# Performance work log

Hardware: AMD Instinct MI355X
Metric: run time of the kernel (lower is better)

The kernel has to match this reference:

```python
import jax, jax.numpy as jnp
import numpy as np

DIM = 384
WIN = 7
HEADS = 12
N = WIN * WIN
B_ = 4096
NW = 64


def _relative_position_index(ws: int) -> np.ndarray:
    coords = np.stack(np.meshgrid(np.arange(ws), np.arange(ws), indexing='ij'))  # (2, ws, ws)
    flat = coords.reshape(2, -1)  # (2, N)
    rel = flat[:, :, None] - flat[:, None, :]  # (2, N, N)
    rel = rel.transpose(1, 2, 0).copy()  # (N, N, 2)
    rel[:, :, 0] += ws - 1
    rel[:, :, 1] += ws - 1
    rel[:, :, 0] *= 2 * ws - 1
    return rel.sum(-1).astype(np.int32)  # (N, N)


def setup_inputs() -> dict:
    key = jax.random.key(0)
    ks = jax.random.split(key, 6)
    x = jax.random.normal(ks[0], (B_, N, DIM), dtype=jnp.float32)
    mask = jnp.zeros((NW, N, N), dtype=jnp.float32)
    bias_table = 0.02 * jax.random.normal(ks[1], ((2 * WIN - 1) ** 2, HEADS), dtype=jnp.float32)
    qkv_w = jax.random.normal(ks[2], (3 * DIM, DIM), dtype=jnp.float32) / np.sqrt(DIM)
    qkv_b = jnp.zeros((3 * DIM,), dtype=jnp.float32)
    proj_w = jax.random.normal(ks[3], (DIM, DIM), dtype=jnp.float32) / np.sqrt(DIM)
    proj_b = jnp.zeros((DIM,), dtype=jnp.float32)
    rel_index = jnp.asarray(_relative_position_index(WIN))  # (N, N) int32
    return {"x": x, "mask": mask, "bias_table": bias_table, "qkv_w": qkv_w,
            "qkv_b": qkv_b, "proj_w": proj_w, "proj_b": proj_b, "rel_index": rel_index}


def reference(x, mask, bias_table, qkv_w, qkv_b, proj_w, proj_b, rel_index):
    Bw, n, c = x.shape
    h = bias_table.shape[1]
    d = c // h
    scale = d ** (-0.5)
    # qkv projection: (Bw, n, 3, h, d)
    qkv = (x @ qkv_w.T + qkv_b).reshape(Bw, n, 3, h, d)
    qkv = jnp.transpose(qkv, (2, 0, 3, 1, 4))  # (3, Bw, h, n, d)
    q, k, v = qkv[0], qkv[1], qkv[2]
    attn = jnp.einsum('bhqd,bhkd->bhqk', q * scale, k)  # (Bw, h, n, n)
    bias = bias_table[rel_index]  # (n, n, h)
    attn = attn + jnp.transpose(bias, (2, 0, 1))[None]  # broadcast over Bw
    nW = mask.shape[0]
    attn = attn.reshape(Bw // nW, nW, h, n, n) + mask[None, :, None]
    attn = attn.reshape(Bw, h, n, n)
    attn = jax.nn.softmax(attn, axis=-1)
    out = jnp.einsum('bhqk,bhkd->bhqd', attn, v)  # (Bw, h, n, d)
    out = jnp.transpose(out, (0, 2, 1, 3)).reshape(Bw, n, c)
    return out @ proj_w.T + proj_b
```

## Files before the change

### kernel.cpp

```cpp
#include <hip/hip_runtime.h>
#include <hip/hip_bf16.h>

#define DIM   384
#define NWIN  49
#define HEADS 12
#define SCALE 0.17677669529663687f

typedef unsigned short ushort;
using bf16x8 = __attribute__((ext_vector_type(8))) short;
using u16x4  = __attribute__((ext_vector_type(4))) ushort;
using f32x4  = __attribute__((ext_vector_type(4))) float;

__device__ __forceinline__ ushort f2bf(float f) {
  unsigned u = __float_as_uint(f);
  u += 0x7fff + ((u >> 16) & 1);
  return (ushort)(u >> 16);
}

typedef __attribute__((address_space(1))) const void gas_void;
typedef __attribute__((address_space(3))) void las_void;

__device__ __forceinline__ void gload16(const ushort* g, ushort* l) {
  __builtin_amdgcn_global_load_lds((gas_void*)g, (las_void*)l, 16, 0, 0);
}

__global__ void prep_kernel(const float* __restrict__ qkv_w, const float* __restrict__ proj_w,
                            const float* __restrict__ bias_table, const int* __restrict__ rel_index,
                            const float* __restrict__ mask, const float* __restrict__ qkv_b,
                            ushort* __restrict__ wqb, ushort* __restrict__ wpb,
                            float* __restrict__ qbF, float* __restrict__ bmF) {
  int i0 = blockIdx.x * 256 + threadIdx.x;
  int stride = gridDim.x * 256;
  for (int i = i0; i < 1152 * 384; i += stride) {
    float v = qkv_w[i];
    if (i < 384 * 384) v *= SCALE;
    wqb[i] = f2bf(v);
  }
  for (int i = i0; i < 384 * 384; i += stride) wpb[i] = f2bf(proj_w[i]);
  for (int i = i0; i < 1152; i += stride) qbF[i] = qkv_b[i] * (i < 384 ? SCALE : 1.f);
  for (int i = i0; i < 64 * HEADS * 4 * 4 * 64 * 4; i += stride) {
    int r = i & 3, lane = (i >> 2) & 63, kt = (i >> 8) & 3, wq = (i >> 10) & 3;
    int hw = i >> 12;
    int h = hw % HEADS, wdx = hw / HEADS;
    int q = wq * 16 + (lane >> 4) * 4 + r;
    int key = kt * 16 + (lane & 15);
    float v;
    if (q < NWIN)
      v = (key < NWIN) ? bias_table[rel_index[q * NWIN + key] * HEADS + h]
                         + mask[wdx * (NWIN * NWIN) + q * NWIN + key]
                       : -3.0e38f;
    else
      v = 0.f;
    bmF[i] = v;
  }
}

#define WB_OFF 0
#define QS_OFF 24576
#define KS_OFF 29440
#define VT_OFF 34304
#define SMEM2_US 39040

__global__ __launch_bounds__(512, 2) void qkv_attn_kernel(
    const float* __restrict__ x, const float* __restrict__ qbF,
    const ushort* __restrict__ wqb, const float* __restrict__ bmF,
    ushort* __restrict__ aog)
{
  extern __shared__ ushort smem[];
  ushort* wb = smem + WB_OFF;

  const int blk = blockIdx.x;
  const int tid = threadIdx.x;
  const int w = tid >> 6, l = tid & 63;
  const int c = l & 15, g = l >> 4;
  const int wm = w >> 1, wn = w & 1;
  const int win = w >> 2, wq = w & 3;
  const float LOG2E = 1.4426950408889634f;

  auto stage_qkv = [&](int h, int kc, int buf) {
    #pragma unroll
    for (int s = 0; s < 3; ++s) {
      int i = s * 512 + tid;
      int n = i >> 4, g16 = i & 15;
      int grow = (n >> 5) * 384 + h * 32 + (n & 31);
      int sg = (g16 & 8) | ((g16 & 7) ^ (n & 7));
      gload16(wqb + (size_t)grow * DIM + kc * 128 + (sg << 3),
              wb + buf * 12288 + i * 8);
    }
  };

  bf16x8 areg[2][12] = {};
  auto compute_qkv = [&](int kcC, int buf, f32x4 (&acc)[2][3]) {
    const ushort* wcb = wb + buf * 12288;
    #pragma unroll
    for (int kk = 0; kk < 4; ++kk) {
      int sB = ((kk * 4 + g) ^ (c & 7)) << 3;
      #pragma unroll
      for (int nt = 0; nt < 3; ++nt) {
        int n = (wn * 3 + nt) * 16 + c;
        bf16x8 bb = *(const bf16x8*)&wcb[n * 128 + sB];
        acc[0][nt] = __builtin_amdgcn_mfma_f32_16x16x32_bf16(areg[0][kcC * 4 + kk], bb, acc[0][nt], 0, 0, 0);
        acc[1][nt] = __builtin_amdgcn_mfma_f32_16x16x32_bf16(areg[1][kcC * 4 + kk], bb, acc[1][nt], 0, 0, 0);
      }
    }
  };

  #pragma unroll
  for (int wi = 0; wi < 2; ++wi) {
    const float* xb = x + (size_t)((blk << 1) + wi) * (NWIN * DIM);
    for (int i = tid; i < 4704; i += 512) {
      float4 f = ((const float4*)xb)[i];
      int row = i / 96, c4 = i - row * 96;
      u16x4 v4 = { f2bf(f.x), f2bf(f.y), f2bf(f.z), f2bf(f.w) };
      *(u16x4*)&wb[row * 384 + c4 * 4] = v4;
    }
    __syncthreads();
    #pragma unroll
    for (int mt = 0; mt < 2; ++mt) {
      int row = wm * 32 + mt * 16 + c;
      int tok = row & 63;
      if ((row >> 6) == wi && tok < NWIN) {
        #pragma unroll
        for (int kg = 0; kg < 12; ++kg)
          areg[mt][kg] = *(const bf16x8*)&wb[tok * 384 + kg * 32 + g * 8];
      }
    }
    __syncthreads();
  }
  stage_qkv(0, 0, 0);
  stage_qkv(0, 1, 1);
  __syncthreads();

  for (int h = 0; h < HEADS; ++h) {
    f32x4 acc[2][3] = {};
    const int par = h & 1;

    compute_qkv(0, par, acc);
    __syncthreads();
    stage_qkv(h, 2, par);

    compute_qkv(1, par ^ 1, acc);
    __syncthreads();
    if (h < 11) stage_qkv(h + 1, 0, par ^ 1);

    compute_qkv(2, par, acc);
    __syncthreads();
    if (h < 11) stage_qkv(h + 1, 1, par);

    {
      int winE = wm >> 1;
      ushort* qsE = smem + QS_OFF + winE * 2432;
      ushort* ksE = smem + KS_OFF + winE * 2432;
      ushort* vtE = smem + VT_OFF + winE * 2368;
      #pragma unroll
      for (int nt = 0; nt < 3; ++nt) {
        int gnt = wn * 3 + nt;
        int which = gnt >> 1;
        int d = (gnt & 1) * 16 + c;
        float qb_ = qbF[which * 384 + h * 32 + d];
        #pragma unroll
        for (int mt = 0; mt < 2; ++mt) {
          #pragma unroll
          for (int r = 0; r < 4; ++r) {
            int tok = (wm & 1) * 32 + mt * 16 + g * 4 + r;
            float v = acc[mt][nt][r] + qb_;
            if (which == 0)      qsE[tok * 38 + d] = f2bf(v);
            else if (which == 1) ksE[tok * 38 + d] = f2bf(v);
            else                 vtE[d * 74 + tok] = f2bf(v);
          }
        }
      }
    }
    __syncthreads();

    ushort* qsw = smem + QS_OFF + win * 2432;
    ushort* ksw = smem + KS_OFF + win * 2432;
    ushort* vtw = smem + VT_OFF + win * 2368;
    const int wdx = ((blk << 1) + win) & 63;
    const f32x4* bw4 = (const f32x4*)(bmF + ((((size_t)(wdx * HEADS + h)) * 4 + wq) * 4 * 64 + l) * 4);
    f32x4 bmv[4];
    #pragma unroll
    for (int kt = 0; kt < 4; ++kt) bmv[kt] = bw4[kt * 64];

    f32x4 sacc[4] = {};
    {
      bf16x8 aq = *(const bf16x8*)&qsw[(wq * 16 + c) * 38 + g * 8];
      #pragma unroll
      for (int kt = 0; kt < 4; ++kt) {
        bf16x8 bk = *(const bf16x8*)&ksw[(kt * 16 + c) * 38 + g * 8];
        sacc[kt] = __builtin_amdgcn_mfma_f32_16x16x32_bf16(aq, bk, sacc[kt], 0, 0, 0);
      }
    }
    float p[4][4];
    #pragma unroll
    for (int r = 0; r < 4; ++r) {
      float s0 = sacc[0][r] + bmv[0][r], s1 = sacc[1][r] + bmv[1][r];
      float s2 = sacc[2][r] + bmv[2][r], s3 = sacc[3][r] + bmv[3][r];
      float mx = fmaxf(fmaxf(s0, s1), fmaxf(s2, s3));
      mx = fmaxf(mx, __shfl_xor(mx, 1, 64));
      mx = fmaxf(mx, __shfl_xor(mx, 2, 64));
      mx = fmaxf(mx, __shfl_xor(mx, 4, 64));
      mx = fmaxf(mx, __shfl_xor(mx, 8, 64));
      float p0 = __builtin_exp2f((s0 - mx) * LOG2E);
      float p1 = __builtin_exp2f((s1 - mx) * LOG2E);
      float p2 = __builtin_exp2f((s2 - mx) * LOG2E);
      float p3 = __builtin_exp2f((s3 - mx) * LOG2E);
      float sum = p0 + p1 + p2 + p3;
      sum += __shfl_xor(sum, 1, 64);
      sum += __shfl_xor(sum, 2, 64);
      sum += __shfl_xor(sum, 4, 64);
      sum += __shfl_xor(sum, 8, 64);
      float inv = 1.0f / sum;
      p[0][r] = p0 * inv; p[1][r] = p1 * inv; p[2][r] = p2 * inv; p[3][r] = p3 * inv;
    }
    f32x4 pacc[2] = {};
    #pragma unroll
    for (int kkh = 0; kkh < 2; ++kkh) {
      #pragma unroll
      for (int t = 0; t < 2; ++t) {
        int kt = kkh * 2 + t;
        #pragma unroll
        for (int r = 0; r < 4; ++r)
          qsw[(wq * 16 + g * 4 + r) * 38 + t * 16 + c] = f2bf(p[kt][r]);
      }
      bf16x8 ap = *(const bf16x8*)&qsw[(wq * 16 + c) * 38 + g * 8];
      #pragma unroll
      for (int dt = 0; dt < 2; ++dt) {
        bf16x8 bv = *(const bf16x8*)&vtw[(dt * 16 + c) * 74 + kkh * 32 + g * 8];
        pacc[dt] = __builtin_amdgcn_mfma_f32_16x16x32_bf16(ap, bv, pacc[dt], 0, 0, 0);
      }
    }
    #pragma unroll
    for (int dt = 0; dt < 2; ++dt) {
      #pragma unroll
      for (int rr = 0; rr < 4; ++rr) {
        int tok = wq * 16 + g * 4 + rr;
        if (tok < NWIN)
          aog[((size_t)((blk << 1) + win) * NWIN + tok) * DIM + h * 32 + dt * 16 + c] =
              f2bf(pacc[dt][rr]);
      }
    }
    __syncthreads();
  }
}

__global__ __launch_bounds__(256, 2) void proj_kernel(
    const ushort* __restrict__ ao, const ushort* __restrict__ wpb,
    const float* __restrict__ proj_b, float* __restrict__ out)
{
  extern __shared__ ushort sm3[];
  ushort* lA = sm3;
  ushort* lB = sm3 + 16384;

  const int blk = blockIdx.x;
  const int bM = blk / 3, bN = blk - bM * 3;
  const int m0 = bM * 128, n0 = bN * 128;
  const int tid = threadIdx.x;
  const int w = tid >> 6, l = tid & 63;
  const int c = l & 15, g = l >> 4;
  const int wm = w >> 1, wn = w & 1;

  auto stageA = [&](int kc, int buf) {
    #pragma unroll
    for (int s = 0; s < 4; ++s) {
      int i = s * 256 + tid;
      int row = i >> 3, g16 = i & 7;
      gload16(ao + (size_t)(m0 + row) * DIM + kc * 64 + ((g16 ^ (row & 7)) << 3),
              lA + buf * 8192 + i * 8);
    }
  };
  auto stageB = [&](int kc, int buf) {
    #pragma unroll
    for (int s = 0; s < 4; ++s) {
      int i = s * 256 + tid;
      int row = i >> 3, g16 = i & 7;
      gload16(wpb + (size_t)(n0 + row) * DIM + kc * 64 + ((g16 ^ (row & 7)) << 3),
              lB + buf * 8192 + i * 8);
    }
  };

  f32x4 acc[4][4] = {};
  stageA(0, 0); stageB(0, 0);
  stageA(1, 1); stageB(1, 1);
  __syncthreads();

  for (int kc = 0; kc < 6; ++kc) {
    const ushort* A = lA + (kc & 1) * 8192;
    const ushort* B = lB + (kc & 1) * 8192;
    #pragma unroll
    for (int kk = 0; kk < 2; ++kk) {
      int swz = ((kk * 4 + g) ^ (c & 7)) << 3;
      bf16x8 af[4], bfr[4];
      #pragma unroll
      for (int mt = 0; mt < 4; ++mt)
        af[mt] = *(const bf16x8*)&A[(wm * 64 + mt * 16 + c) * 64 + swz];
      #pragma unroll
      for (int nt = 0; nt < 4; ++nt)
        bfr[nt] = *(const bf16x8*)&B[(wn * 64 + nt * 16 + c) * 64 + swz];
      #pragma unroll
      for (int mt = 0; mt < 4; ++mt)
        #pragma unroll
        for (int nt = 0; nt < 4; ++nt)
          acc[mt][nt] = __builtin_amdgcn_mfma_f32_16x16x32_bf16(af[mt], bfr[nt], acc[mt][nt], 0, 0, 0);
    }
    __syncthreads();
    if (kc + 2 < 6) { stageA(kc + 2, kc & 1); stageB(kc + 2, kc & 1); }
  }

  #pragma unroll
  for (int nt = 0; nt < 4; ++nt) {
    int col = n0 + wn * 64 + nt * 16 + c;
    float pb = proj_b[col];
    #pragma unroll
    for (int mt = 0; mt < 4; ++mt) {
      #pragma unroll
      for (int r = 0; r < 4; ++r) {
        int row = m0 + wm * 64 + mt * 16 + g * 4 + r;
        out[(size_t)row * DIM + col] = acc[mt][nt][r] + pb;
      }
    }
  }
}

#define FWB_OFF 0
#define FQS_OFF 24576
#define FKS_OFF 29696
#define FVT_OFF 34816
#define FAO_OFF 39424
#define FSMEM_US 77056

__global__ __launch_bounds__(512, 2) void winattn_fused(
    const float* __restrict__ x, const float* __restrict__ qbF,
    const float* __restrict__ proj_b, const ushort* __restrict__ wqb,
    const ushort* __restrict__ wpb, const float* __restrict__ bmF,
    float* __restrict__ out)
{
  extern __shared__ ushort smem[];
  ushort* wb = smem + FWB_OFF;
  ushort* ao = smem + FAO_OFF;

  const int blk = blockIdx.x;
  const int tid = threadIdx.x;
  const int w = tid >> 6, l = tid & 63;
  const int c = l & 15, g = l >> 4;
  const int wm = w >> 1, wn = w & 1;
  const int win = w >> 2, wq = w & 3;
  const float LOG2E = 1.4426950408889634f;

  ushort* qsw = smem + FQS_OFF + win * 2560;
  ushort* ksw = smem + FKS_OFF + win * 2560;
  ushort* vtw = smem + FVT_OFF + win * 2304;
  ushort* psw = qsw;

  auto stage_qkv = [&](int h, int kc, int buf) {
    #pragma unroll
    for (int s = 0; s < 3; ++s) {
      int i = s * 512 + tid;
      int n = i >> 4, g16 = i & 15;
      int grow = (n >> 5) * 384 + h * 32 + (n & 31);
      int sg = (g16 & 8) | ((g16 & 7) ^ (n & 7));
      gload16(wqb + (size_t)grow * DIM + kc * 128 + (sg << 3), wb + buf * 12288 + i * 8);
    }
  };
  auto stage_proj = [&](int nb, int kc, int buf) {
    #pragma unroll
    for (int s = 0; s < 3; ++s) {
      int i = s * 512 + tid;
      int n = i >> 4, g16 = i & 15;
      int grow = nb * 96 + n;
      int sg = (g16 & 8) | ((g16 & 7) ^ (n & 7));
      gload16(wpb + (size_t)grow * DIM + kc * 128 + (sg << 3), wb + buf * 12288 + i * 8);
    }
  };

  bf16x8 areg[2][12] = {};
  auto compute_qkv = [&](int kcC, int buf, f32x4 (&acc)[2][3]) {
    const ushort* wcb = wb + buf * 12288;
    #pragma unroll
    for (int kk = 0; kk < 4; ++kk) {
      int sB = ((kk * 4 + g) ^ (c & 7)) << 3;
      #pragma unroll
      for (int nt = 0; nt < 3; ++nt) {
        int n = (wn * 3 + nt) * 16 + c;
        bf16x8 bb = *(const bf16x8*)&wcb[n * 128 + sB];
        acc[0][nt] = __builtin_amdgcn_mfma_f32_16x16x32_bf16(areg[0][kcC * 4 + kk], bb, acc[0][nt], 0, 0, 0);
        acc[1][nt] = __builtin_amdgcn_mfma_f32_16x16x32_bf16(areg[1][kcC * 4 + kk], bb, acc[1][nt], 0, 0, 0);
      }
    }
  };
  auto compute_proj = [&](int kcC, int buf, f32x4 (&acc)[2][3]) {
    const ushort* wcb = wb + buf * 12288;
    int r0 = wm * 32 + c;      if (r0 >= 98) r0 -= 64;
    int r1 = wm * 32 + 16 + c; if (r1 >= 98) r1 -= 64;
    #pragma unroll
    for (int kk = 0; kk < 4; ++kk) {
      int p = kcC * 16 + kk * 4 + g;
      int sw = (p ^ (c & 7)) << 3;
      bf16x8 a0 = *(const bf16x8*)&ao[r0 * 384 + sw];
      bf16x8 a1 = *(const bf16x8*)&ao[r1 * 384 + sw];
      int sB = ((kk * 4 + g) ^ (c & 7)) << 3;
      #pragma unroll
      for (int nt = 0; nt < 3; ++nt) {
        int n = (wn * 3 + nt) * 16 + c;
        bf16x8 bb = *(const bf16x8*)&wcb[n * 128 + sB];
        acc[0][nt] = __builtin_amdgcn_mfma_f32_16x16x32_bf16(a0, bb, acc[0][nt], 0, 0, 0);
        acc[1][nt] = __builtin_amdgcn_mfma_f32_16x16x32_bf16(a1, bb, acc[1][nt], 0, 0, 0);
      }
    }
  };

  stage_qkv(0, 0, 0);
  stage_qkv(0, 1, 1);
  {
    const float* xb = x + (size_t)blk * (2 * NWIN * DIM);
    for (int i = tid; i < 9408; i += 512) {
      float4 f = ((const float4*)xb)[i];
      int row = i / 96, c4 = i - row * 96;
      int k = c4 * 4;
      int gr = k >> 3;
      u16x4 v4 = { f2bf(f.x), f2bf(f.y), f2bf(f.z), f2bf(f.w) };
      *(u16x4*)&ao[row * 384 + ((gr ^ (row & 7)) << 3) + (k & 7)] = v4;
    }
  }
  __syncthreads();
  #pragma unroll
  for (int mt = 0; mt < 2; ++mt) {
    int row = wm * 32 + mt * 16 + c;
    int wi = row >> 6, tok = row & 63;
    if (tok < NWIN) {
      int ar = wi * 49 + tok;
      #pragma unroll
      for (int kg = 0; kg < 12; ++kg)
        areg[mt][kg] = *(const bf16x8*)&ao[ar * 384 + (((kg * 4 + g) ^ (ar & 7)) << 3)];
    }
  }

  for (int h = 0; h < HEADS; ++h) {
    f32x4 acc[2][3] = {};
    const int par = h & 1;
    compute_qkv(0, par, acc);
    __syncthreads();
    stage_qkv(h, 2, par);
    compute_qkv(1, par ^ 1, acc);
    __syncthreads();
    if (h < 11) stage_qkv(h + 1, 0, par ^ 1); else stage_proj(0, 0, par ^ 1);
    compute_qkv(2, par, acc);
    __syncthreads();
    if (h < 11) stage_qkv(h + 1, 1, par); else stage_proj(0, 1, par);
    {
      int winE = wm >> 1;
      ushort* qsE = smem + FQS_OFF + winE * 2560;
      ushort* ksE = smem + FKS_OFF + winE * 2560;
      ushort* vtE = smem + FVT_OFF + winE * 2304;
      #pragma unroll
      for (int nt = 0; nt < 3; ++nt) {
        int gnt = wn * 3 + nt;
        int which = gnt >> 1;
        int d = (gnt & 1) * 16 + c;
        float qb_ = qbF[which * 384 + h * 32 + d];
        #pragma unroll
        for (int mt = 0; mt < 2; ++mt) {
          #pragma unroll
          for (int r = 0; r < 4; ++r) {
            int tok = (wm & 1) * 32 + mt * 16 + g * 4 + r;
            float v = acc[mt][nt][r] + qb_;
            if (which == 0)      qsE[tok * 40 + d] = f2bf(v);
            else if (which == 1) ksE[tok * 40 + d] = f2bf(v);
            else                 vtE[d * 72 + tok] = f2bf(v);
          }
        }
      }
    }
    __syncthreads();

    const int wdx = ((blk << 1) + win) & 63;
    const f32x4* bw4 = (const f32x4*)(bmF + ((((size_t)(wdx * HEADS + h)) * 4 + wq) * 4 * 64 + l) * 4);
    f32x4 bmv[4];
    #pragma unroll
    for (int kt = 0; kt < 4; ++kt) bmv[kt] = bw4[kt * 64];

    f32x4 sacc[4] = {};
    {
      bf16x8 aq = *(const bf16x8*)&qsw[(wq * 16 + c) * 40 + g * 8];
      #pragma unroll
      for (int kt = 0; kt < 4; ++kt) {
        bf16x8 bk = *(const bf16x8*)&ksw[(kt * 16 + c) * 40 + g * 8];
        sacc[kt] = __builtin_amdgcn_mfma_f32_16x16x32_bf16(aq, bk, sacc[kt], 0, 0, 0);
      }
    }
    float p[4][4];
    #pragma unroll
    for (int r = 0; r < 4; ++r) {
      float s0 = sacc[0][r] + bmv[0][r], s1 = sacc[1][r] + bmv[1][r];
      float s2 = sacc[2][r] + bmv[2][r], s3 = sacc[3][r] + bmv[3][r];
      float mx = fmaxf(fmaxf(s0, s1), fmaxf(s2, s3));
      mx = fmaxf(mx, __shfl_xor(mx, 1, 64));
      mx = fmaxf(mx, __shfl_xor(mx, 2, 64));
      mx = fmaxf(mx, __shfl_xor(mx, 4, 64));
      mx = fmaxf(mx, __shfl_xor(mx, 8, 64));
      float p0 = __builtin_exp2f((s0 - mx) * LOG2E);
      float p1 = __builtin_exp2f((s1 - mx) * LOG2E);
      float p2 = __builtin_exp2f((s2 - mx) * LOG2E);
      float p3 = __builtin_exp2f((s3 - mx) * LOG2E);
      float sum = p0 + p1 + p2 + p3;
      sum += __shfl_xor(sum, 1, 64);
      sum += __shfl_xor(sum, 2, 64);
      sum += __shfl_xor(sum, 4, 64);
      sum += __shfl_xor(sum, 8, 64);
      float inv = 1.0f / sum;
      p[0][r] = p0 * inv; p[1][r] = p1 * inv; p[2][r] = p2 * inv; p[3][r] = p3 * inv;
    }
    f32x4 pacc2[2] = {};
    #pragma unroll
    for (int kkh = 0; kkh < 2; ++kkh) {
      #pragma unroll
      for (int t = 0; t < 2; ++t) {
        int kt = kkh * 2 + t;
        #pragma unroll
        for (int r = 0; r < 4; ++r)
          psw[(wq * 16 + g * 4 + r) * 40 + t * 16 + c] = f2bf(p[kt][r]);
      }
      bf16x8 ap = *(const bf16x8*)&psw[(wq * 16 + c) * 40 + g * 8];
      #pragma unroll
      for (int dt = 0; dt < 2; ++dt) {
        bf16x8 bv = *(const bf16x8*)&vtw[(dt * 16 + c) * 72 + kkh * 32 + g * 8];
        pacc2[dt] = __builtin_amdgcn_mfma_f32_16x16x32_bf16(ap, bv, pacc2[dt], 0, 0, 0);
      }
    }
    #pragma unroll
    for (int dt = 0; dt < 2; ++dt) {
      int gr0 = h * 4 + dt * 2 + (c >> 3);
      #pragma unroll
      for (int rr = 0; rr < 4; ++rr) {
        int tok = wq * 16 + g * 4 + rr;
        int row0 = win * 49 + tok;
        if (tok < NWIN)
          ao[row0 * 384 + (((gr0 ^ (row0 & 7)) << 3) | (c & 7))] = f2bf(pacc2[dt][rr]);
      }
    }
    __syncthreads();
  }

  __syncthreads();
  for (int nb = 0; nb < 4; ++nb) {
    f32x4 acc[2][3] = {};
    const int pb0 = (nb * 3) & 1;
    compute_proj(0, pb0, acc);
    __syncthreads();
    stage_proj(nb, 2, pb0);
    compute_proj(1, pb0 ^ 1, acc);
    __syncthreads();
    if (nb < 3) stage_proj(nb + 1, 0, pb0 ^ 1);
    compute_proj(2, pb0, acc);
    __syncthreads();
    if (nb < 3) stage_proj(nb + 1, 1, pb0);
    #pragma unroll
    for (int nt = 0; nt < 3; ++nt) {
      int col = nb * 96 + (wn * 3 + nt) * 16 + c;
      float pb = proj_b[col];
      #pragma unroll
      for (int mt = 0; mt < 2; ++mt) {
        #pragma unroll
        for (int r = 0; r < 4; ++r) {
          int mrow = wm * 32 + mt * 16 + g * 4 + r;
          if (mrow < 98) {
            int wi = mrow >= NWIN;
            int tok = mrow - (wi ? NWIN : 0);
            out[((size_t)((blk << 1) + wi) * NWIN + tok) * DIM + col] = acc[mt][nt][r] + pb;
          }
        }
      }
    }
  }
}

extern "C" void kernel_launch(void* const* d_in, const int* in_sizes, int n_in,
                              void* d_out, int out_size, void* d_ws, size_t ws_size,
                              hipStream_t stream) {
  const float* x          = (const float*)d_in[0];
  const float* mask       = (const float*)d_in[1];
  const float* bias_table = (const float*)d_in[2];
  const float* qkv_w      = (const float*)d_in[3];
  const float* qkv_b      = (const float*)d_in[4];
  const float* proj_w     = (const float*)d_in[5];
  const float* proj_b     = (const float*)d_in[6];
  const int*   rel_index  = (const int*)d_in[7];
  float* out = (float*)d_out;

  ushort* wqb = (ushort*)d_ws;
  ushort* wpb = (ushort*)((char*)d_ws + 884736);
  float*  qbF = (float*)((char*)d_ws + 1179648);
  float*  bmF = (float*)((char*)d_ws + 1184256);
  ushort* aog = (ushort*)((char*)d_ws + 13767168);
  const size_t NEED = 13767168ull + 154140672ull;

  prep_kernel<<<1024, 256, 0, stream>>>(qkv_w, proj_w, bias_table, rel_index, mask, qkv_b,
                                        wqb, wpb, qbF, bmF);

  if (ws_size >= NEED) {
    hipFuncSetAttribute((const void*)qkv_attn_kernel,
                        hipFuncAttributeMaxDynamicSharedMemorySize, SMEM2_US * 2);
    qkv_attn_kernel<<<2048, 512, SMEM2_US * 2, stream>>>(x, qbF, wqb, bmF, aog);
    hipFuncSetAttribute((const void*)proj_kernel,
                        hipFuncAttributeMaxDynamicSharedMemorySize, 65536);
    proj_kernel<<<4704, 256, 65536, stream>>>(aog, wpb, proj_b, out);
  } else {
    hipFuncSetAttribute((const void*)winattn_fused,
                        hipFuncAttributeMaxDynamicSharedMemorySize, FSMEM_US * 2);
    winattn_fused<<<2048, 512, FSMEM_US * 2, stream>>>(x, qbF, proj_b, wqb, wpb, bmF, out);
  }
}
```

Measured before the change: 937.6 us.

## Split fused QKV+attention into separate QKV GEMM, attention, and projection kernels

Result: no change. 929.7 us (-0.8%).

```diff
diff --git a/kernel.cpp b/kernel.cpp
--- a/kernel.cpp
+++ b/kernel.cpp
@@ -55,19 +55,295 @@
   }
 }
 
-#define WB_OFF 0
-#define QS_OFF 24576
-#define KS_OFF 29440
-#define VT_OFF 34304
-#define SMEM2_US 39040
-
-__global__ __launch_bounds__(512, 2) void qkv_attn_kernel(
+__global__ __launch_bounds__(256) void qkv_gemm_kernel(
     const float* __restrict__ x, const float* __restrict__ qbF,
-    const ushort* __restrict__ wqb, const float* __restrict__ bmF,
-    ushort* __restrict__ aog)
+    const ushort* __restrict__ wqb,
+    ushort* __restrict__ qg, ushort* __restrict__ kg, ushort* __restrict__ vg)
+{
+  extern __shared__ ushort smA[];
+  ushort* lA = smA;
+  ushort* lB = smA + 16384;
+
+  const int blk = blockIdx.x;
+  const int bM = blk / 9, bN = blk - bM * 9;
+  const int m0 = bM * 128, n0 = bN * 128;
+  const int which = bN / 3;
+  ushort* outw = which == 0 ? qg : (which == 1 ? kg : vg);
+  const int tid = threadIdx.x;
+  const int w = tid >> 6, l = tid & 63;
+  const int c = l & 15, g = l >> 4;
+  const int wm = w >> 1, wn = w & 1;
+
+  auto stageA = [&](int kc, int buf) {
+    #pragma unroll
+    for (int s = 0; s < 4; ++s) {
+      int i = s * 256 + tid;
+      int row = i >> 3, gc = i & 7;
+      const float4* src = (const float4*)(x + (size_t)(m0 + row) * DIM + kc * 64 + gc * 8);
+      float4 f0 = src[0], f1 = src[1];
+      ushort tmp[8] = { f2bf(f0.x), f2bf(f0.y), f2bf(f0.z), f2bf(f0.w),
+                        f2bf(f1.x), f2bf(f1.y), f2bf(f1.z), f2bf(f1.w) };
+      *(bf16x8*)&lA[buf * 8192 + row * 64 + ((gc ^ (row & 7)) << 3)] = *(bf16x8*)tmp;
+    }
+  };
+  auto stageB = [&](int kc, int buf) {
+    #pragma unroll
+    for (int s = 0; s < 4; ++s) {
+      int i = s * 256 + tid;
+      int row = i >> 3, gc = i & 7;
+      gload16(wqb + (size_t)(n0 + row) * DIM + kc * 64 + ((gc ^ (row & 7)) << 3),
+              lB + buf * 8192 + i * 8);
+    }
+  };
+
+  f32x4 acc[4][4] = {};
+  stageA(0, 0); stageB(0, 0);
+  stageA(1, 1); stageB(1, 1);
+  __syncthreads();
+
+  for (int kc = 0; kc < 6; ++kc) {
+    const ushort* A = lA + (kc & 1) * 8192;
+    const ushort* B = lB + (kc & 1) * 8192;
+    #pragma unroll
+    for (int kk = 0; kk < 2; ++kk) {
+      int swz = ((kk * 4 + g) ^ (c & 7)) << 3;
+      bf16x8 af[4], bfr[4];
+      #pragma unroll
+      for (int mt = 0; mt < 4; ++mt)
+        af[mt] = *(const bf16x8*)&A[(wm * 64 + mt * 16 + c) * 64 + swz];
+      #pragma unroll
+      for (int nt = 0; nt < 4; ++nt)
+        bfr[nt] = *(const bf16x8*)&B[(wn * 64 + nt * 16 + c) * 64 + swz];
+      #pragma unroll
+      for (int mt = 0; mt < 4; ++mt)
+        #pragma unroll
+        for (int nt = 0; nt < 4; ++nt)
+          acc[mt][nt] = __builtin_amdgcn_mfma_f32_16x16x32_bf16(af[mt], bfr[nt], acc[mt][nt], 0, 0, 0);
+    }
+    __syncthreads();
+    if (kc + 2 < 6) { stageA(kc + 2, kc & 1); stageB(kc + 2, kc & 1); }
+  }
+
+  #pragma unroll
+  for (int nt = 0; nt < 4; ++nt) {
+    int n = n0 + wn * 64 + nt * 16 + c;
+    int h = (n - which * 384) >> 5;
+    int d = n & 31;
+    float qb_ = qbF[n];
+    #pragma unroll
+    for (int mt = 0; mt < 4; ++mt) {
+      #pragma unroll
+      for (int r = 0; r < 4; ++r) {
+        int tok = m0 + wm * 64 + mt * 16 + g * 4 + r;
+        int win = tok / 49;
+        int tk = tok - win * 49;
+        outw[((size_t)(win * HEADS + h) * NWIN + tk) * 32 + d] = f2bf(acc[mt][nt][r] + qb_);
+      }
+    }
+  }
+}
+
+#define VSTR 68
+__global__ __launch_bounds__(256) void attn_kernel(
+    const ushort* __restrict__ kg, const ushort* __restrict__ vg,
+    const float* __restrict__ bmF, ushort* __restrict__ qg)
+{
+  __shared__ ushort vts[4][32 * VSTR];
+  __shared__ ushort pbs[4][16 * 36];
+
+  const int tid = threadIdx.x;
+  const int w = tid >> 6, l = tid & 63;
+  const int c = l & 15, g = l >> 4;
+  const int task = blockIdx.x * 4 + w;
+  const int win = task / 12, h = task - win * 12;
+  const int wdx = win & 63;
+  const float LOG2E = 1.4426950408889634f;
+
+  const size_t sb = (size_t)(win * HEADS + h) * (NWIN * 32);
+  ushort* qslice = qg + sb;
+  const ushort* kb = kg + sb;
+  const ushort* vb = vg + sb;
+  ushort* vt = vts[w];
+  ushort* pb = pbs[w];
+
+  bf16x8 qf[4], kf[4];
+  #pragma unroll
+  for (int t = 0; t < 4; ++t) {
+    qf[t] = *(const bf16x8*)(qslice + (t * 16 + c) * 32 + g * 8);
+    kf[t] = *(const bf16x8*)(kb + (t * 16 + c) * 32 + g * 8);
+  }
+  #pragma unroll
+  for (int it = 0; it < 25; ++it) {
+    int i = it * 64 + l;
+    if (i < NWIN * 32) vt[(i & 31) * VSTR + (i >> 5)] = vb[i];
+  }
+  for (int i = l; i < 32 * 15; i += 64) {
+    int d = i / 15, t = NWIN + (i - d * 15);
+    vt[d * VSTR + t] = 0;
+  }
+
+  const float* bmBase = bmF + (size_t)((wdx * HEADS + h) * 4) * 1024 + l * 4;
+
+  #pragma unroll
+  for (int qt = 0; qt < 4; ++qt) {
+    f32x4 sacc[4] = {};
+    #pragma unroll
+    for (int kt = 0; kt < 4; ++kt)
+      sacc[kt] = __builtin_amdgcn_mfma_f32_16x16x32_bf16(qf[qt], kf[kt], sacc[kt], 0, 0, 0);
+    const f32x4* bw4 = (const f32x4*)(bmBase + qt * 1024);
+    float p[4][4];
+    {
+      f32x4 b0 = bw4[0], b1 = bw4[64], b2 = bw4[128], b3 = bw4[192];
+      #pragma unroll
+      for (int r = 0; r < 4; ++r) {
+        float s0 = sacc[0][r] + b0[r], s1 = sacc[1][r] + b1[r];
+        float s2 = sacc[2][r] + b2[r], s3 = sacc[3][r] + b3[r];
+        float mx = fmaxf(fmaxf(s0, s1), fmaxf(s2, s3));
+        mx = fmaxf(mx, __shfl_xor(mx, 1, 64));
+        mx = fmaxf(mx, __shfl_xor(mx, 2, 64));
+        mx = fmaxf(mx, __shfl_xor(mx, 4, 64));
+        mx = fmaxf(mx, __shfl_xor(mx, 8, 64));
+        float p0 = __builtin_exp2f((s0 - mx) * LOG2E);
+        float p1 = __builtin_exp2f((s1 - mx) * LOG2E);
+        float p2 = __builtin_exp2f((s2 - mx) * LOG2E);
+        float p3 = __builtin_exp2f((s3 - mx) * LOG2E);
+        float sum = p0 + p1 + p2 + p3;
+        sum += __shfl_xor(sum, 1, 64);
+        sum += __shfl_xor(sum, 2, 64);
+        sum += __shfl_xor(sum, 4, 64);
+        sum += __shfl_xor(sum, 8, 64);
+        float inv = 1.0f / sum;
+        p[0][r] = p0 * inv; p[1][r] = p1 * inv; p[2][r] = p2 * inv; p[3][r] = p3 * inv;
+      }
+    }
+    f32x4 pacc[2] = {};
+    #pragma unroll
+    for (int kkh = 0; kkh < 2; ++kkh) {
+      #pragma unroll
+      for (int t = 0; t < 2; ++t) {
+        int kt = kkh * 2 + t;
+        #pragma unroll
+        for (int r = 0; r < 4; ++r)
+          pb[(g * 4 + r) * 36 + t * 16 + c] = f2bf(p[kt][r]);
+      }
+      bf16x8 ap = *(const bf16x8*)&pb[c * 36 + g * 8];
+      #pragma unroll
+      for (int dt = 0; dt < 2; ++dt) {
+        bf16x8 bv = *(const bf16x8*)&vt[(dt * 16 + c) * VSTR + kkh * 32 + g * 8];
+        pacc[dt] = __builtin_amdgcn_mfma_f32_16x16x32_bf16(ap, bv, pacc[dt], 0, 0, 0);
+      }
+    }
+    #pragma unroll
+    for (int dt = 0; dt < 2; ++dt) {
+      #pragma unroll
+      for (int rr = 0; rr < 4; ++rr) {
+        int tok = qt * 16 + g * 4 + rr;
+        if (tok < NWIN)
+          qslice[tok * 32 + dt * 16 + c] = f2bf(pacc[dt][rr]);
+      }
+    }
+  }
+}
+
+__global__ __launch_bounds__(256, 2) void proj_kernel(
+    const ushort* __restrict__ ao, const ushort* __restrict__ wpb,
+    const float* __restrict__ proj_b, float* __restrict__ out)
+{
+  extern __shared__ ushort sm3[];
+  ushort* lA = sm3;
+  ushort* lB = sm3 + 16384;
+
+  const int blk = blockIdx.x;
+  const int bM = blk / 3, bN = blk - bM * 3;
+  const int m0 = bM * 128, n0 = bN * 128;
+  const int tid = threadIdx.x;
+  const int w = tid >> 6, l = tid & 63;
+  const int c = l & 15, g = l >> 4;
+  const int wm = w >> 1, wn = w & 1;
+
+  auto stageA = [&](int kc, int buf) {
+    #pragma unroll
+    for (int s = 0; s < 4; ++s) {
+      int i = s * 256 + tid;
+      int row = i >> 3, gc = i & 7;
+      int tok = m0 + row;
+      int win = tok / 49;
+      int tk = tok - win * 49;
+      int sg = gc ^ (row & 7);
+      int kfull = kc * 64 + sg * 8;
+      gload16(ao + ((size_t)(win * HEADS + (kfull >> 5)) * NWIN + tk) * 32 + (kfull & 31),
+              lA + buf * 8192 + i * 8);
+    }
+  };
+  auto stageB = [&](int kc, int buf) {
+    #pragma unroll
+    for (int s = 0; s < 4; ++s) {
+      int i = s * 256 + tid;
+      int row = i >> 3, gc = i & 7;
+      gload16(wpb + (size_t)(n0 + row) * DIM + kc * 64 + ((gc ^ (row & 7)) << 3),
+              lB + buf * 8192 + i * 8);
+    }
+  };
+
+  f32x4 acc[4][4] = {};
+  stageA(0, 0); stageB(0, 0);
+  stageA(1, 1); stageB(1, 1);
+  __syncthreads();
+
+  for (int kc = 0; kc < 6; ++kc) {
+    const ushort* A = lA + (kc & 1) * 8192;
+    const ushort* B = lB + (kc & 1) * 8192;
+    #pragma unroll
+    for (int kk = 0; kk < 2; ++kk) {
+      int swz = ((kk * 4 + g) ^ (c & 7)) << 3;
+      bf16x8 af[4], bfr[4];
+      #pragma unroll
+      for (int mt = 0; mt < 4; ++mt)
+        af[mt] = *(const bf16x8*)&A[(wm * 64 + mt * 16 + c) * 64 + swz];
+      #pragma unroll
+      for (int nt = 0; nt < 4; ++nt)
+        bfr[nt] = *(const bf16x8*)&B[(wn * 64 + nt * 16 + c) * 64 + swz];
+      #pragma unroll
+      for (int mt = 0; mt < 4; ++mt)
+        #pragma unroll
+        for (int nt = 0; nt < 4; ++nt)
+          acc[mt][nt] = __builtin_amdgcn_mfma_f32_16x16x32_bf16(af[mt], bfr[nt], acc[mt][nt], 0, 0, 0);
+    }
+    __syncthreads();
+    if (kc + 2 < 6) { stageA(kc + 2, kc & 1); stageB(kc + 2, kc & 1); }
+  }
+
+  #pragma unroll
+  for (int nt = 0; nt < 4; ++nt) {
+    int col = n0 + wn * 64 + nt * 16 + c;
+    float pb = proj_b[col];
+    #pragma unroll
+    for (int mt = 0; mt < 4; ++mt) {
+      #pragma unroll
+      for (int r = 0; r < 4; ++r) {
+        int row = m0 + wm * 64 + mt * 16 + g * 4 + r;
+        out[(size_t)row * DIM + col] = acc[mt][nt][r] + pb;
+      }
+    }
+  }
+}
+
+#define FWB_OFF 0
+#define FQS_OFF 24576
+#define FKS_OFF 29696
+#define FVT_OFF 34816
+#define FAO_OFF 39424
+#define FSMEM_US 77056
+
+__global__ __launch_bounds__(512, 2) void winattn_fused(
+    const float* __restrict__ x, const float* __restrict__ qbF,
+    const float* __restrict__ proj_b, const ushort* __restrict__ wqb,
+    const ushort* __restrict__ wpb, const float* __restrict__ bmF,
+    float* __restrict__ out)
 {
   extern __shared__ ushort smem[];
-  ushort* wb = smem + WB_OFF;
+  ushort* wb = smem + FWB_OFF;
+  ushort* ao = smem + FAO_OFF;
 
   const int blk = blockIdx.x;
   const int tid = threadIdx.x;
@@ -77,6 +353,11 @@
   const int win = w >> 2, wq = w & 3;
   const float LOG2E = 1.4426950408889634f;
 
+  ushort* qsw = smem + FQS_OFF + win * 2560;
+  ushort* ksw = smem + FKS_OFF + win * 2560;
+  ushort* vtw = smem + FVT_OFF + win * 2304;
+  ushort* psw = qsw;
+
   auto stage_qkv = [&](int h, int kc, int buf) {
     #pragma unroll
     for (int s = 0; s < 3; ++s) {
@@ -84,8 +365,17 @@
       int n = i >> 4, g16 = i & 15;
       int grow = (n >> 5) * 384 + h * 32 + (n & 31);
       int sg = (g16 & 8) | ((g16 & 7) ^ (n & 7));
-      gload16(wqb + (size_t)grow * DIM + kc * 128 + (sg << 3),
-              wb + buf * 12288 + i * 8);
+      gload16(wqb + (size_t)grow * DIM + kc * 128 + (sg << 3), wb + buf * 12288 + i * 8);
+    }
+  };
+  auto stage_proj = [&](int nb, int kc, int buf) {
+    #pragma unroll
+    for (int s = 0; s < 3; ++s) {
+      int i = s * 512 + tid;
+      int n = i >> 4, g16 = i & 15;
+      int grow = nb * 96 + n;
+      int sg = (g16 & 8) | ((g16 & 7) ^ (n & 7));
+      gload16(wpb + (size_t)grow * DIM + kc * 128 + (sg << 3), wb + buf * 12288 + i * 8);
     }
   };
 
@@ -104,54 +394,70 @@
       }
     }
   };
-
-  #pragma unroll
-  for (int wi = 0; wi < 2; ++wi) {
-    const float* xb = x + (size_t)((blk << 1) + wi) * (NWIN * DIM);
-    for (int i = tid; i < 4704; i += 512) {
+  auto compute_proj = [&](int kcC, int buf, f32x4 (&acc)[2][3]) {
+    const ushort* wcb = wb + buf * 12288;
+    int r0 = wm * 32 + c;      if (r0 >= 98) r0 -= 64;
+    int r1 = wm * 32 + 16 + c; if (r1 >= 98) r1 -= 64;
+    #pragma unroll
+    for (int kk = 0; kk < 4; ++kk) {
+      int p = kcC * 16 + kk * 4 + g;
+      int sw = (p ^ (c & 7)) << 3;
+      bf16x8 a0 = *(const bf16x8*)&ao[r0 * 384 + sw];
+      bf16x8 a1 = *(const bf16x8*)&ao[r1 * 384 + sw];
+      int sB = ((kk * 4 + g) ^ (c & 7)) << 3;
+      #pragma unroll
+      for (int nt = 0; nt < 3; ++nt) {
+        int n = (wn * 3 + nt) * 16 + c;
+        bf16x8 bb = *(const bf16x8*)&wcb[n * 128 + sB];
+        acc[0][nt] = __builtin_amdgcn_mfma_f32_16x16x32_bf16(a0, bb, acc[0][nt], 0, 0, 0);
+        acc[1][nt] = __builtin_amdgcn_mfma_f32_16x16x32_bf16(a1, bb, acc[1][nt], 0, 0, 0);
+      }
+    }
+  };
+
+  stage_qkv(0, 0, 0);
+  stage_qkv(0, 1, 1);
+  {
+    const float* xb = x + (size_t)blk * (2 * NWIN * DIM);
+    for (int i = tid; i < 9408; i += 512) {
       float4 f = ((const float4*)xb)[i];
       int row = i / 96, c4 = i - row * 96;
+      int k = c4 * 4;
+      int gr = k >> 3;
       u16x4 v4 = { f2bf(f.x), f2bf(f.y), f2bf(f.z), f2bf(f.w) };
-      *(u16x4*)&wb[row * 384 + c4 * 4] = v4;
-    }
-    __syncthreads();
-    #pragma unroll
-    for (int mt = 0; mt < 2; ++mt) {
-      int row = wm * 32 + mt * 16 + c;
-      int tok = row & 63;
-      if ((row >> 6) == wi && tok < NWIN) {
-        #pragma unroll
-        for (int kg = 0; kg < 12; ++kg)
-          areg[mt][kg] = *(const bf16x8*)&wb[tok * 384 + kg * 32 + g * 8];
-      }
-    }
-    __syncthreads();
-  }
-  stage_qkv(0, 0, 0);
-  stage_qkv(0, 1, 1);
+      *(u16x4*)&ao[row * 384 + ((gr ^ (row & 7)) << 3) + (k & 7)] = v4;
+    }
+  }
   __syncthreads();
+  #pragma unroll
+  for (int mt = 0; mt < 2; ++mt) {
+    int row = wm * 32 + mt * 16 + c;
+    int wi = row >> 6, tok = row & 63;
+    if (tok < NWIN) {
+      int ar = wi * 49 + tok;
+      #pragma unroll
+      for (int kg = 0; kg < 12; ++kg)
+        areg[mt][kg] = *(const bf16x8*)&ao[ar * 384 + (((kg * 4 + g) ^ (ar & 7)) << 3)];
+    }
+  }
 
   for (int h = 0; h < HEADS; ++h) {
     f32x4 acc[2][3] = {};
     const int par = h & 1;
-
     compute_qkv(0, par, acc);
     __syncthreads();
     stage_qkv(h, 2, par);
-
     compute_qkv(1, par ^ 1, acc);
     __syncthreads();
-    if (h < 11) stage_qkv(h + 1, 0, par ^ 1);
-
+    if (h < 11) stage_qkv(h + 1, 0, par ^ 1); else stage_proj(0, 0, par ^ 1);
     compute_qkv(2, par, acc);
     __syncthreads();
-    if (h < 11) stage_qkv(h + 1, 1, par);
-
+    if (h < 11) stage_qkv(h + 1, 1, par); else stage_proj(0, 1, par);
     {
       int winE = wm >> 1;
-      ushort* qsE = smem + QS_OFF + winE * 2432;
-      ushort* ksE = smem + KS_OFF + winE * 2432;
-      ushort* vtE = smem + VT_OFF + winE * 2368;
+      ushort* qsE = smem + FQS_OFF + winE * 2560;
+      ushort* ksE = smem + FKS_OFF + winE * 2560;
+      ushort* vtE = smem + FVT_OFF + winE * 2304;
       #pragma unroll
       for (int nt = 0; nt < 3; ++nt) {
         int gnt = wn * 3 + nt;
@@ -164,18 +470,15 @@
           for (int r = 0; r < 4; ++r) {
             int tok = (wm & 1) * 32 + mt * 16 + g * 4 + r;
             float v = acc[mt][nt][r] + qb_;
-            if (which == 0)      qsE[tok * 38 + d] = f2bf(v);
-            else if (which == 1) ksE[tok * 38 + d] = f2bf(v);
-            else                 vtE[d * 74 + tok] = f2bf(v);
+            if (which == 0)      qsE[tok * 40 + d] = f2bf(v);
+            else if (which == 1) ksE[tok * 40 + d] = f2bf(v);
+            else                 vtE[d * 72 + tok] = f2bf(v);
           }
         }
       }
     }
     __syncthreads();
 
-    ushort* qsw = smem + QS_OFF + win * 2432;
-    ushort* ksw = smem + KS_OFF + win * 2432;
-    ushort* vtw = smem + VT_OFF + win * 2368;
     const int wdx = ((blk << 1) + win) & 63;
     const f32x4* bw4 = (const f32x4*)(bmF + ((((size_t)(wdx * HEADS + h)) * 4 + wq) * 4 * 64 + l) * 4);
     f32x4 bmv[4];
@@ -184,10 +487,10 @@
 
     f32x4 sacc[4] = {};
     {
-      bf16x8 aq = *(const bf16x8*)&qsw[(wq * 16 + c) * 38 + g * 8];
+      bf16x8 aq = *(const bf16x8*)&qsw[(wq * 16 + c) * 40 + g * 8];
       #pragma unroll
       for (int kt = 0; kt < 4; ++kt) {
-        bf16x8 bk = *(const bf16x8*)&ksw[(kt * 16 + c) * 38 + g * 8];
+        bf16x8 bk = *(const bf16x8*)&ksw[(kt * 16 + c) * 40 + g * 8];
         sacc[kt] = __builtin_amdgcn_mfma_f32_16x16x32_bf16(aq, bk, sacc[kt], 0, 0, 0);
       }
     }
@@ -213,303 +516,6 @@
       float inv = 1.0f / sum;
       p[0][r] = p0 * inv; p[1][r] = p1 * inv; p[2][r] = p2 * inv; p[3][r] = p3 * inv;
     }
-    f32x4 pacc[2] = {};
-    #pragma unroll
-    for (int kkh = 0; kkh < 2; ++kkh) {
-      #pragma unroll
-      for (int t = 0; t < 2; ++t) {
-        int kt = kkh * 2 + t;
-        #pragma unroll
-        for (int r = 0; r < 4; ++r)
-          qsw[(wq * 16 + g * 4 + r) * 38 + t * 16 + c] = f2bf(p[kt][r]);
-      }
-      bf16x8 ap = *(const bf16x8*)&qsw[(wq * 16 + c) * 38 + g * 8];
-      #pragma unroll
-      for (int dt = 0; dt < 2; ++dt) {
-        bf16x8 bv = *(const bf16x8*)&vtw[(dt * 16 + c) * 74 + kkh * 32 + g * 8];
-        pacc[dt] = __builtin_amdgcn_mfma_f32_16x16x32_bf16(ap, bv, pacc[dt], 0, 0, 0);
-      }
-    }
-    #pragma unroll
-    for (int dt = 0; dt < 2; ++dt) {
-      #pragma unroll
-      for (int rr = 0; rr < 4; ++rr) {
-        int tok = wq * 16 + g * 4 + rr;
-        if (tok < NWIN)
-          aog[((size_t)((blk << 1) + win) * NWIN + tok) * DIM + h * 32 + dt * 16 + c] =
-              f2bf(pacc[dt][rr]);
-      }
-    }
-    __syncthreads();
-  }
-}
-
-__global__ __launch_bounds__(256, 2) void proj_kernel(
-    const ushort* __restrict__ ao, const ushort* __restrict__ wpb,
-    const float* __restrict__ proj_b, float* __restrict__ out)
-{
-  extern __shared__ ushort sm3[];
-  ushort* lA = sm3;
-  ushort* lB = sm3 + 16384;
-
-  const int blk = blockIdx.x;
-  const int bM = blk / 3, bN = blk - bM * 3;
-  const int m0 = bM * 128, n0 = bN * 128;
-  const int tid = threadIdx.x;
-  const int w = tid >> 6, l = tid & 63;
-  const int c = l & 15, g = l >> 4;
-  const int wm = w >> 1, wn = w & 1;
-
-  auto stageA = [&](int kc, int buf) {
-    #pragma unroll
-    for (int s = 0; s < 4; ++s) {
-      int i = s * 256 + tid;
-      int row = i >> 3, g16 = i & 7;
-      gload16(ao + (size_t)(m0 + row) * DIM + kc * 64 + ((g16 ^ (row & 7)) << 3),
-              lA + buf * 8192 + i * 8);
-    }
-  };
-  auto stageB = [&](int kc, int buf) {
-    #pragma unroll
-    for (int s = 0; s < 4; ++s) {
-      int i = s * 256 + tid;
-      int row = i >> 3, g16 = i & 7;
-      gload16(wpb + (size_t)(n0 + row) * DIM + kc * 64 + ((g16 ^ (row & 7)) << 3),
-              lB + buf * 8192 + i * 8);
-    }
-  };
-
-  f32x4 acc[4][4] = {};
-  stageA(0, 0); stageB(0, 0);
-  stageA(1, 1); stageB(1, 1);
-  __syncthreads();
-
-  for (int kc = 0; kc < 6; ++kc) {
-    const ushort* A = lA + (kc & 1) * 8192;
-    const ushort* B = lB + (kc & 1) * 8192;
-    #pragma unroll
-    for (int kk = 0; kk < 2; ++kk) {
-      int swz = ((kk * 4 + g) ^ (c & 7)) << 3;
-      bf16x8 af[4], bfr[4];
-      #pragma unroll
-      for (int mt = 0; mt < 4; ++mt)
-        af[mt] = *(const bf16x8*)&A[(wm * 64 + mt * 16 + c) * 64 + swz];
-      #pragma unroll
-      for (int nt = 0; nt < 4; ++nt)
-        bfr[nt] = *(const bf16x8*)&B[(wn * 64 + nt * 16 + c) * 64 + swz];
-      #pragma unroll
-      for (int mt = 0; mt < 4; ++mt)
-        #pragma unroll
-        for (int nt = 0; nt < 4; ++nt)
-          acc[mt][nt] = __builtin_amdgcn_mfma_f32_16x16x32_bf16(af[mt], bfr[nt], acc[mt][nt], 0, 0, 0);
-    }
-    __syncthreads();
-    if (kc + 2 < 6) { stageA(kc + 2, kc & 1); stageB(kc + 2, kc & 1); }
-  }
-
-  #pragma unroll
-  for (int nt = 0; nt < 4; ++nt) {
-    int col = n0 + wn * 64 + nt * 16 + c;
-    float pb = proj_b[col];
-    #pragma unroll
-    for (int mt = 0; mt < 4; ++mt) {
-      #pragma unroll
-      for (int r = 0; r < 4; ++r) {
-        int row = m0 + wm * 64 + mt * 16 + g * 4 + r;
-        out[(size_t)row * DIM + col] = acc[mt][nt][r] + pb;
-      }
-    }
-  }
-}
-
-#define FWB_OFF 0
-#define FQS_OFF 24576
-#define FKS_OFF 29696
-#define FVT_OFF 34816
-#define FAO_OFF 39424
-#define FSMEM_US 77056
-
-__global__ __launch_bounds__(512, 2) void winattn_fused(
-    const float* __restrict__ x, const float* __restrict__ qbF,
-    const float* __restrict__ proj_b, const ushort* __restrict__ wqb,
-    const ushort* __restrict__ wpb, const float* __restrict__ bmF,
-    float* __restrict__ out)
-{
-  extern __shared__ ushort smem[];
-  ushort* wb = smem + FWB_OFF;
-  ushort* ao = smem + FAO_OFF;
-
-  const int blk = blockIdx.x;
-  const int tid = threadIdx.x;
-  const int w = tid >> 6, l = tid & 63;
-  const int c = l & 15, g = l >> 4;
-  const int wm = w >> 1, wn = w & 1;
-  const int win = w >> 2, wq = w & 3;
-  const float LOG2E = 1.4426950408889634f;
-
-  ushort* qsw = smem + FQS_OFF + win * 2560;
-  ushort* ksw = smem + FKS_OFF + win * 2560;
-  ushort* vtw = smem + FVT_OFF + win * 2304;
-  ushort* psw = qsw;
-
-  auto stage_qkv = [&](int h, int kc, int buf) {
-    #pragma unroll
-    for (int s = 0; s < 3; ++s) {
-      int i = s * 512 + tid;
-      int n = i >> 4, g16 = i & 15;
-      int grow = (n >> 5) * 384 + h * 32 + (n & 31);
-      int sg = (g16 & 8) | ((g16 & 7) ^ (n & 7));
-      gload16(wqb + (size_t)grow * DIM + kc * 128 + (sg << 3), wb + buf * 12288 + i * 8);
-    }
-  };
-  auto stage_proj = [&](int nb, int kc, int buf) {
-    #pragma unroll
-    for (int s = 0; s < 3; ++s) {
-      int i = s * 512 + tid;
-      int n = i >> 4, g16 = i & 15;
-      int grow = nb * 96 + n;
-      int sg = (g16 & 8) | ((g16 & 7) ^ (n & 7));
-      gload16(wpb + (size_t)grow * DIM + kc * 128 + (sg << 3), wb + buf * 12288 + i * 8);
-    }
-  };
-
-  bf16x8 areg[2][12] = {};
-  auto compute_qkv = [&](int kcC, int buf, f32x4 (&acc)[2][3]) {
-    const ushort* wcb = wb + buf * 12288;
-    #pragma unroll
-    for (int kk = 0; kk < 4; ++kk) {
-      int sB = ((kk * 4 + g) ^ (c & 7)) << 3;
-      #pragma unroll
-      for (int nt = 0; nt < 3; ++nt) {
-        int n = (wn * 3 + nt) * 16 + c;
-        bf16x8 bb = *(const bf16x8*)&wcb[n * 128 + sB];
-        acc[0][nt] = __builtin_amdgcn_mfma_f32_16x16x32_bf16(areg[0][kcC * 4 + kk], bb, acc[0][nt], 0, 0, 0);
-        acc[1][nt] = __builtin_amdgcn_mfma_f32_16x16x32_bf16(areg[1][kcC * 4 + kk], bb, acc[1][nt], 0, 0, 0);
-      }
-    }
-  };
-  auto compute_proj = [&](int kcC, int buf, f32x4 (&acc)[2][3]) {
-    const ushort* wcb = wb + buf * 12288;
-    int r0 = wm * 32 + c;      if (r0 >= 98) r0 -= 64;
-    int r1 = wm * 32 + 16 + c; if (r1 >= 98) r1 -= 64;
-    #pragma unroll
-    for (int kk = 0; kk < 4; ++kk) {
-      int p = kcC * 16 + kk * 4 + g;
-      int sw = (p ^ (c & 7)) << 3;
-      bf16x8 a0 = *(const bf16x8*)&ao[r0 * 384 + sw];
-      bf16x8 a1 = *(const bf16x8*)&ao[r1 * 384 + sw];
-      int sB = ((kk * 4 + g) ^ (c & 7)) << 3;
-      #pragma unroll
-      for (int nt = 0; nt < 3; ++nt) {
-        int n = (wn * 3 + nt) * 16 + c;
-        bf16x8 bb = *(const bf16x8*)&wcb[n * 128 + sB];
-        acc[0][nt] = __builtin_amdgcn_mfma_f32_16x16x32_bf16(a0, bb, acc[0][nt], 0, 0, 0);
-        acc[1][nt] = __builtin_amdgcn_mfma_f32_16x16x32_bf16(a1, bb, acc[1][nt], 0, 0, 0);
-      }
-    }
-  };
-
-  stage_qkv(0, 0, 0);
-  stage_qkv(0, 1, 1);
-  {
-    const float* xb = x + (size_t)blk * (2 * NWIN * DIM);
-    for (int i = tid; i < 9408; i += 512) {
-      float4 f = ((const float4*)xb)[i];
-      int row = i / 96, c4 = i - row * 96;
-      int k = c4 * 4;
-      int gr = k >> 3;
-      u16x4 v4 = { f2bf(f.x), f2bf(f.y), f2bf(f.z), f2bf(f.w) };
-      *(u16x4*)&ao[row * 384 + ((gr ^ (row & 7)) << 3) + (k & 7)] = v4;
-    }
-  }
-  __syncthreads();
-  #pragma unroll
-  for (int mt = 0; mt < 2; ++mt) {
-    int row = wm * 32 + mt * 16 + c;
-    int wi = row >> 6, tok = row & 63;
-    if (tok < NWIN) {
-      int ar = wi * 49 + tok;
-      #pragma unroll
-      for (int kg = 0; kg < 12; ++kg)
-        areg[mt][kg] = *(const bf16x8*)&ao[ar * 384 + (((kg * 4 + g) ^ (ar & 7)) << 3)];
-    }
-  }
-
-  for (int h = 0; h < HEADS; ++h) {
-    f32x4 acc[2][3] = {};
-    const int par = h & 1;
-    compute_qkv(0, par, acc);
-    __syncthreads();
-    stage_qkv(h, 2, par);
-    compute_qkv(1, par ^ 1, acc);
-    __syncthreads();
-    if (h < 11) stage_qkv(h + 1, 0, par ^ 1); else stage_proj(0, 0, par ^ 1);
-    compute_qkv(2, par, acc);
-    __syncthreads();
-    if (h < 11) stage_qkv(h + 1, 1, par); else stage_proj(0, 1, par);
-    {
-      int winE = wm >> 1;
-      ushort* qsE = smem + FQS_OFF + winE * 2560;
-      ushort* ksE = smem + FKS_OFF + winE * 2560;
-      ushort* vtE = smem + FVT_OFF + winE * 2304;
-      #pragma unroll
-      for (int nt = 0; nt < 3; ++nt) {
-        int gnt = wn * 3 + nt;
-        int which = gnt >> 1;
-        int d = (gnt & 1) * 16 + c;
-        float qb_ = qbF[which * 384 + h * 32 + d];
-        #pragma unroll
-        for (int mt = 0; mt < 2; ++mt) {
-          #pragma unroll
-          for (int r = 0; r < 4; ++r) {
-            int tok = (wm & 1) * 32 + mt * 16 + g * 4 + r;
-            float v = acc[mt][nt][r] + qb_;
-            if (which == 0)      qsE[tok * 40 + d] = f2bf(v);
-            else if (which == 1) ksE[tok * 40 + d] = f2bf(v);
-            else                 vtE[d * 72 + tok] = f2bf(v);
-          }
-        }
-      }
-    }
-    __syncthreads();
-
-    const int wdx = ((blk << 1) + win) & 63;
-    const f32x4* bw4 = (const f32x4*)(bmF + ((((size_t)(wdx * HEADS + h)) * 4 + wq) * 4 * 64 + l) * 4);
-    f32x4 bmv[4];
-    #pragma unroll
-    for (int kt = 0; kt < 4; ++kt) bmv[kt] = bw4[kt * 64];
-
-    f32x4 sacc[4] = {};
-    {
-      bf16x8 aq = *(const bf16x8*)&qsw[(wq * 16 + c) * 40 + g * 8];
-      #pragma unroll
-      for (int kt = 0; kt < 4; ++kt) {
-        bf16x8 bk = *(const bf16x8*)&ksw[(kt * 16 + c) * 40 + g * 8];
-        sacc[kt] = __builtin_amdgcn_mfma_f32_16x16x32_bf16(aq, bk, sacc[kt], 0, 0, 0);
-      }
-    }
-    float p[4][4];
-    #pragma unroll
-    for (int r = 0; r < 4; ++r) {
-      float s0 = sacc[0][r] + bmv[0][r], s1 = sacc[1][r] + bmv[1][r];
-      float s2 = sacc[2][r] + bmv[2][r], s3 = sacc[3][r] + bmv[3][r];
-      float mx = fmaxf(fmaxf(s0, s1), fmaxf(s2, s3));
-      mx = fmaxf(mx, __shfl_xor(mx, 1, 64));
-      mx = fmaxf(mx, __shfl_xor(mx, 2, 64));
-      mx = fmaxf(mx, __shfl_xor(mx, 4, 64));
-      mx = fmaxf(mx, __shfl_xor(mx, 8, 64));
-      float p0 = __builtin_exp2f((s0 - mx) * LOG2E);
-      float p1 = __builtin_exp2f((s1 - mx) * LOG2E);
-      float p2 = __builtin_exp2f((s2 - mx) * LOG2E);
-      float p3 = __builtin_exp2f((s3 - mx) * LOG2E);
-      float sum = p0 + p1 + p2 + p3;
-      sum += __shfl_xor(sum, 1, 64);
-      sum += __shfl_xor(sum, 2, 64);
-      sum += __shfl_xor(sum, 4, 64);
-      sum += __shfl_xor(sum, 8, 64);
-      float inv = 1.0f / sum;
-      p[0][r] = p0 * inv; p[1][r] = p1 * inv; p[2][r] = p2 * inv; p[3][r] = p3 * inv;
-    }
     f32x4 pacc2[2] = {};
     #pragma unroll
     for (int kkh = 0; kkh < 2; ++kkh) {
@@ -591,19 +597,22 @@
   ushort* wpb = (ushort*)((char*)d_ws + 884736);
   float*  qbF = (float*)((char*)d_ws + 1179648);
   float*  bmF = (float*)((char*)d_ws + 1184256);
-  ushort* aog = (ushort*)((char*)d_ws + 13767168);
-  const size_t NEED = 13767168ull + 154140672ull;
+  ushort* qg  = (ushort*)((char*)d_ws + 13767168);
+  ushort* kg  = (ushort*)((char*)d_ws + 167907840);
+  ushort* vg  = (ushort*)((char*)d_ws + 322048512);
+  const size_t NEED = 476189184ull;
 
   prep_kernel<<<1024, 256, 0, stream>>>(qkv_w, proj_w, bias_table, rel_index, mask, qkv_b,
                                         wqb, wpb, qbF, bmF);
 
   if (ws_size >= NEED) {
-    hipFuncSetAttribute((const void*)qkv_attn_kernel,
-                        hipFuncAttributeMaxDynamicSharedMemorySize, SMEM2_US * 2);
-    qkv_attn_kernel<<<2048, 512, SMEM2_US * 2, stream>>>(x, qbF, wqb, bmF, aog);
+    hipFuncSetAttribute((const void*)qkv_gemm_kernel,
+                        hipFuncAttributeMaxDynamicSharedMemorySize, 65536);
+    qkv_gemm_kernel<<<14112, 256, 65536, stream>>>(x, qbF, wqb, qg, kg, vg);
+    attn_kernel<<<12288, 256, 0, stream>>>(kg, vg, bmF, qg);
     hipFuncSetAttribute((const void*)proj_kernel,
                         hipFuncAttributeMaxDynamicSharedMemorySize, 65536);
-    proj_kernel<<<4704, 256, 65536, stream>>>(aog, wpb, proj_b, out);
+    proj_kernel<<<4704, 256, 65536, stream>>>(qg, wpb, proj_b, out);
   } else {
     hipFuncSetAttribute((const void*)winattn_fused,
                         hipFuncAttributeMaxDynamicSharedMemorySize, FSMEM_US * 2);
```
